# Optimization experiments

Hardware: AMD Instinct MI355X
Metric: run time of the kernel (lower is better)

## Reference

```python
import jax, jax.numpy as jnp
import numpy as np

EMBED = 1024
HEADS = 16
HEAD_DIM = EMBED // HEADS
N, S = 2, 2048


def setup_inputs() -> dict:
    key0 = jax.random.key(0)
    ks = jax.random.split(key0, 9)
    inp = {
        "value": jax.random.normal(ks[0], (N, S, EMBED), dtype=jnp.float32),
        "key": jax.random.normal(ks[1], (N, S, EMBED), dtype=jnp.float32),
        "query": jax.random.normal(ks[2], (N, S, EMBED), dtype=jnp.float32),
        "mask": jax.random.randint(ks[3], (N, 1, S, S), 0, 2, dtype=jnp.int32),
        # per-head projection weights (nn.Linear: y = x @ W.T), bias=False
        "Wv": jax.random.normal(ks[4], (HEAD_DIM, HEAD_DIM), dtype=jnp.float32) / np.sqrt(HEAD_DIM),
        "Wk": jax.random.normal(ks[5], (HEAD_DIM, HEAD_DIM), dtype=jnp.float32) / np.sqrt(HEAD_DIM),
        "Wq": jax.random.normal(ks[6], (HEAD_DIM, HEAD_DIM), dtype=jnp.float32) / np.sqrt(HEAD_DIM),
        "Wo": jax.random.normal(ks[7], (EMBED, EMBED), dtype=jnp.float32) / np.sqrt(EMBED),
        "bo": jax.random.normal(ks[8], (EMBED,), dtype=jnp.float32) * 0.01,
    }
    return inp


def reference(value, key, query, mask, Wv, Wk, Wq, Wo, bo):
    n, q_len = query.shape[0], query.shape[1]
    v = value.reshape(n, -1, HEADS, HEAD_DIM)
    k = key.reshape(n, -1, HEADS, HEAD_DIM)
    q = query.reshape(n, -1, HEADS, HEAD_DIM)
    # per-head linear projections (x @ W.T)
    v = jnp.einsum('nlhd,ed->nlhe', v, Wv)
    k = jnp.einsum('nlhd,ed->nlhe', k, Wk)
    q = jnp.einsum('nlhd,ed->nlhe', q, Wq)
    energy = jnp.einsum('nqhd,nkhd->nhqk', q, k)
    # faithful to the source: masked_fill with +1e20 where mask == 0
    energy = jnp.where(mask == 0, jnp.float32(1e20), energy)
    attention = jax.nn.softmax(energy / jnp.sqrt(jnp.float32(EMBED)), axis=3)
    out = jnp.einsum('nhql,nlhd->nqhd', attention, v)
    out = out.reshape(n, q_len, EMBED)
    return out @ Wo.T + bo
```

## Files before the change

kernel.cpp:

```cpp
#include <hip/hip_runtime.h>
#include <hip/hip_bf16.h>
#include <stdint.h>

#define SEQ 2048

typedef __attribute__((ext_vector_type(8))) short s8v;
typedef __attribute__((ext_vector_type(4))) float f4v;
typedef __attribute__((ext_vector_type(4))) int   i4v;

#define QCLIP 5.5f

static __device__ __forceinline__ unsigned short f2bf(float f) {
  union { float f; unsigned u; } x; x.f = f;
  return (unsigned short)((x.u + 0x7FFFu + ((x.u >> 16) & 1u)) >> 16);
}

static __device__ __forceinline__ void glds16(const void* g, void* l) {
  auto* lp = reinterpret_cast<__attribute__((address_space(3))) unsigned int*>(
      reinterpret_cast<uintptr_t>(l));
  const auto* gp = reinterpret_cast<const __attribute__((address_space(1))) unsigned int*>(
      reinterpret_cast<uintptr_t>(g));
  __builtin_amdgcn_global_load_lds(gp, lp, 16, 0, 0);
}

__global__ void k_prep(const float* __restrict__ V, const float* __restrict__ Wv,
                       const float* __restrict__ Wo,
                       unsigned short* __restrict__ Vb, unsigned short* __restrict__ W2t) {
  const int bid = blockIdx.x, tid = threadIdx.x;
  __shared__ float wv_s[64 * 64];
  if (bid < 2048) {
    int t = bid * 256 + tid;
    const float4* src = (const float4*)V;
    float4 a = src[t * 2], b = src[t * 2 + 1];
    ushort4 p0, p1;
    p0.x = f2bf(a.x); p0.y = f2bf(a.y); p0.z = f2bf(a.z); p0.w = f2bf(a.w);
    p1.x = f2bf(b.x); p1.y = f2bf(b.y); p1.z = f2bf(b.z); p1.w = f2bf(b.w);
    ((ushort4*)Vb)[t * 2] = p0; ((ushort4*)Vb)[t * 2 + 1] = p1;
  } else {
    int b = bid - 2048;
#pragma unroll
    for (int i = 0; i < 4; ++i) { int c = tid + i * 256; ((float4*)wv_s)[c] = ((const float4*)Wv)[c]; }
    __syncthreads();
    const int f = b >> 2;
    const int g = ((b & 3) << 8) + tid;
    const int h = g >> 6, dd = g & 63;
    const float* wo = Wo + f * 1024 + h * 64;
    float acc = 0.f;
#pragma unroll
    for (int e = 0; e < 64; ++e) acc += wv_s[e * 64 + dd] * wo[e];
    W2t[(size_t)f * 1024 + g] = f2bf(acc);
  }
}

__global__ __launch_bounds__(256, 2) void k_gemm0m(
    const unsigned short* __restrict__ A, const unsigned short* __restrict__ Bt,
    signed char* __restrict__ Ut8,
    const int* __restrict__ mask, signed char* __restrict__ Mi8,
    float* __restrict__ rcnt) {
  __shared__ __align__(16) unsigned short As[2][64 * 64];
  __shared__ __align__(16) unsigned short Bs[2][128 * 64];
  const int bid = blockIdx.x, tid = threadIdx.x;

  if (bid >= 512) {
    int row = bid - 512;
    const int4* mrow = (const int4*)(mask + (size_t)row * SEQ);
    int4 a = mrow[tid * 2], b = mrow[tid * 2 + 1];
    unsigned lo = (a.x == 0 ? 1u : 0u) | ((a.y == 0 ? 1u : 0u) << 8) |
                  ((a.z == 0 ? 1u : 0u) << 16) | ((a.w == 0 ? 1u : 0u) << 24);
    unsigned hi = (b.x == 0 ? 1u : 0u) | ((b.y == 0 ? 1u : 0u) << 8) |
                  ((b.z == 0 ? 1u : 0u) << 16) | ((b.w == 0 ? 1u : 0u) << 24);
    uint2 pk; pk.x = lo; pk.y = hi;
    *(uint2*)(Mi8 + (size_t)row * SEQ + tid * 8) = pk;
    int* red = (int*)As;
    red[tid] = (a.x == 0) + (a.y == 0) + (a.z == 0) + (a.w == 0)
             + (b.x == 0) + (b.y == 0) + (b.z == 0) + (b.w == 0);
    __syncthreads();
    for (int s = 128; s > 0; s >>= 1) { if (tid < s) red[tid] += red[tid + s]; __syncthreads(); }
    if (tid == 0) rcnt[row] = 1.0f / (float)red[0];
    return;
  }

  const int Kdim = 1024;
  const int wave = tid >> 6, lane = tid & 63;
  const int quad = lane >> 4, l15 = lane & 15;
  const int wm = (wave & 1) * 32, wn = (wave >> 1) * 64;
  const int lg = ((bid & 7) << 6) + (bid >> 3);
  const int bm0 = (lg >> 3) * 64, bn0 = (lg & 7) * 128;

  const int ra = tid >> 3, pa = tid & 7;
  const unsigned short* ga0 = A + (size_t)(bm0 + ra) * Kdim + (pa ^ ((ra >> 1) & 7)) * 8;
  const unsigned short* ga1 = A + (size_t)(bm0 + 32 + ra) * Kdim + (pa ^ (((ra + 32) >> 1) & 7)) * 8;
  const unsigned short* gb[4];
#pragma unroll
  for (int j = 0; j < 4; ++j) {
    int rb = (tid + j * 256) >> 3;
    gb[j] = Bt + (size_t)(bn0 + rb) * Kdim + ((pa ^ ((rb >> 1) & 7))) * 8;
  }

  f4v acc[2][4];
#pragma unroll
  for (int i = 0; i < 2; ++i)
#pragma unroll
    for (int j = 0; j < 4; ++j) acc[i][j] = (f4v){0.f, 0.f, 0.f, 0.f};

  auto stage = [&](int buf, int k) {
    glds16(ga0 + k, As[buf] + tid * 8);
    glds16(ga1 + k, As[buf] + (tid + 256) * 8);
#pragma unroll
    for (int j = 0; j < 4; ++j) glds16(gb[j] + k, Bs[buf] + (tid + j * 256) * 8);
  };
  auto compute = [&](int buf) {
#pragma unroll
    for (int kg = 0; kg < 2; ++kg) {
      const int pos = ((kg * 4 + quad) ^ ((l15 >> 1) & 7)) * 8;
      s8v af[2], bf[4];
#pragma unroll
      for (int t = 0; t < 2; ++t)
        af[t] = *(const s8v*)(As[buf] + (wm + t * 16 + l15) * 64 + pos);
#pragma unroll
      for (int u = 0; u < 4; ++u)
        bf[u] = *(const s8v*)(Bs[buf] + (wn + u * 16 + l15) * 64 + pos);
#pragma unroll
      for (int tm = 0; tm < 2; ++tm)
#pragma unroll
        for (int tn = 0; tn < 4; ++tn)
          acc[tm][tn] = __builtin_amdgcn_mfma_f32_16x16x32_bf16(af[tm], bf[tn], acc[tm][tn], 0, 0, 0);
    }
  };

  stage(0, 0);
  for (int k0 = 0; k0 < Kdim; k0 += 128) {
    __syncthreads();
    if (k0 + 64 < Kdim) stage(1, k0 + 64);
    compute(0);
    __syncthreads();
    if (k0 + 128 < Kdim) stage(0, k0 + 128);
    compute(1);
  }

  const float qs = 127.0f / QCLIP;
#pragma unroll
  for (int tm = 0; tm < 2; ++tm)
#pragma unroll
    for (int tn = 0; tn < 4; ++tn) {
      int gm0 = bm0 + wm + tm * 16 + quad * 4;
      int f   = bn0 + wn + tn * 16 + l15;
      int batch = gm0 >> 11, l0 = gm0 & 2047;
      unsigned pk = 0;
#pragma unroll
      for (int r = 0; r < 4; ++r) {
        float v = fminf(fmaxf(acc[tm][tn][r], -QCLIP), QCLIP) * qs;
        int q = __float2int_rn(v);
        pk |= ((unsigned)(q & 255)) << (8 * r);
      }
      *(unsigned*)(Ut8 + (size_t)batch * (1024 * SEQ) + (size_t)f * SEQ + l0) = pk;
    }
}

__global__ __launch_bounds__(256, 2) void k_gemm1(
    const signed char* __restrict__ A,
    const signed char* __restrict__ Bt,
    float* __restrict__ Out,
    const float* __restrict__ rcnt, const float* __restrict__ bo) {
  __shared__ __align__(16) signed char As[2][64 * 128];
  __shared__ __align__(16) signed char Bs[2][128 * 128];
  const int bid = blockIdx.x, tid = threadIdx.x;

  const int lg = ((bid & 7) << 6) + (bid >> 3);
  const int batch = lg >> 8;
  const int rest = lg & 255;
  const int bm0 = (rest >> 3) * 64, bn0 = (rest & 7) * 128;

  A    += (size_t)batch * SEQ * SEQ;
  Bt   += (size_t)batch * 1024 * SEQ;
  rcnt += (size_t)batch * SEQ;
  Out  += (size_t)batch * SEQ * 1024;

  const int wave = tid >> 6, lane = tid & 63;
  const int quad = lane >> 4, l15 = lane & 15;
  const int wm = (wave & 1) * 32, wn = (wave >> 1) * 64;

  const signed char* ga[2];
  const signed char* gb[4];
#pragma unroll
  for (int j = 0; j < 2; ++j) {
    int c = tid + j * 256, r = c >> 3, p = c & 7;
    ga[j] = A + (size_t)(bm0 + r) * SEQ + (p ^ ((r >> 1) & 7)) * 16;
  }
#pragma unroll
  for (int j = 0; j < 4; ++j) {
    int c = tid + j * 256, r = c >> 3, p = c & 7;
    gb[j] = Bt + (size_t)(bn0 + r) * SEQ + (p ^ ((r >> 1) & 7)) * 16;
  }

  i4v acc[2][4];
#pragma unroll
  for (int i = 0; i < 2; ++i)
#pragma unroll
    for (int j = 0; j < 4; ++j) acc[i][j] = (i4v){0, 0, 0, 0};

  auto stage = [&](int buf, int k) {
#pragma unroll
    for (int j = 0; j < 2; ++j)
      glds16(ga[j] + k, As[buf] + (tid + j * 256) * 16);
#pragma unroll
    for (int j = 0; j < 4; ++j)
      glds16(gb[j] + k, Bs[buf] + (tid + j * 256) * 16);
  };
  auto compute = [&](int buf) {
#pragma unroll
    for (int kg = 0; kg < 2; ++kg) {
      const int pos = ((kg * 4 + quad) ^ ((l15 >> 1) & 7)) * 16;
      i4v af[2], bf[4];
#pragma unroll
      for (int t = 0; t < 2; ++t)
        af[t] = *(const i4v*)(As[buf] + (wm + t * 16 + l15) * 128 + pos);
#pragma unroll
      for (int u = 0; u < 4; ++u)
        bf[u] = *(const i4v*)(Bs[buf] + (wn + u * 16 + l15) * 128 + pos);
#pragma unroll
      for (int tm = 0; tm < 2; ++tm)
#pragma unroll
        for (int tn = 0; tn < 4; ++tn)
          acc[tm][tn] = __builtin_amdgcn_mfma_i32_16x16x64_i8(af[tm], bf[tn], acc[tm][tn], 0, 0, 0);
    }
  };

  stage(0, 0);
  for (int k0 = 0; k0 < SEQ; k0 += 256) {
    __syncthreads();
    if (k0 + 128 < SEQ) stage(1, k0 + 128);
    compute(0);
    __syncthreads();
    if (k0 + 256 < SEQ) stage(0, k0 + 256);
    compute(1);
  }

  const float s = QCLIP / 127.0f;
#pragma unroll
  for (int tm = 0; tm < 2; ++tm)
#pragma unroll
    for (int tn = 0; tn < 4; ++tn) {
      int gm0 = bm0 + wm + tm * 16 + quad * 4;
      int f   = bn0 + wn + tn * 16 + l15;
      float bof = bo[f];
#pragma unroll
      for (int r = 0; r < 4; ++r) {
        int row = gm0 + r;
        Out[(size_t)row * 1024 + f] = (float)acc[tm][tn][r] * s * rcnt[row] + bof;
      }
    }
}

extern "C" void kernel_launch(void* const* d_in, const int* in_sizes, int n_in,
                              void* d_out, int out_size, void* d_ws, size_t ws_size,
                              hipStream_t stream) {
  const float* V   = (const float*)d_in[0];
  const int* mask  = (const int*)d_in[3];
  const float* Wv  = (const float*)d_in[4];
  const float* Wo  = (const float*)d_in[7];
  const float* bo  = (const float*)d_in[8];

  char* ws = (char*)d_ws;
  unsigned short* W2t  = (unsigned short*)ws;
  signed char*    Ut8  = (signed char*)(ws + ((size_t)2  << 20));
  unsigned short* Vb   = (unsigned short*)(ws + ((size_t)6  << 20));
  signed char*    Mi8  = (signed char*)(ws + ((size_t)14 << 20));
  float*          rcnt = (float*)(ws + ((size_t)22 << 20));

  k_prep<<<6144, 256, 0, stream>>>(V, Wv, Wo, Vb, W2t);
  k_gemm0m<<<4608, 256, 0, stream>>>(Vb, W2t, Ut8, mask, Mi8, rcnt);
  k_gemm1<<<512, 256, 0, stream>>>(Mi8, Ut8, (float*)d_out, rcnt, bo);
}
```

Measured before the change: 156.7 us.

## Fuse fp32-to-bf16 conversion of V into the GEMM A-tile loading

```diff
diff --git a/kernel.cpp b/kernel.cpp
--- a/kernel.cpp
+++ b/kernel.cpp
@@ -23,37 +23,31 @@
   __builtin_amdgcn_global_load_lds(gp, lp, 16, 0, 0);
 }
 
-__global__ void k_prep(const float* __restrict__ V, const float* __restrict__ Wv,
-                       const float* __restrict__ Wo,
-                       unsigned short* __restrict__ Vb, unsigned short* __restrict__ W2t) {
-  const int bid = blockIdx.x, tid = threadIdx.x;
+__global__ void k_prepW(const float* __restrict__ Wv, const float* __restrict__ Wo,
+                        unsigned short* __restrict__ W2t) {
+  const int f = blockIdx.x, tid = threadIdx.x;
   __shared__ float wv_s[64 * 64];
-  if (bid < 2048) {
-    int t = bid * 256 + tid;
-    const float4* src = (const float4*)V;
-    float4 a = src[t * 2], b = src[t * 2 + 1];
-    ushort4 p0, p1;
-    p0.x = f2bf(a.x); p0.y = f2bf(a.y); p0.z = f2bf(a.z); p0.w = f2bf(a.w);
-    p1.x = f2bf(b.x); p1.y = f2bf(b.y); p1.z = f2bf(b.z); p1.w = f2bf(b.w);
-    ((ushort4*)Vb)[t * 2] = p0; ((ushort4*)Vb)[t * 2 + 1] = p1;
-  } else {
-    int b = bid - 2048;
-#pragma unroll
-    for (int i = 0; i < 4; ++i) { int c = tid + i * 256; ((float4*)wv_s)[c] = ((const float4*)Wv)[c]; }
-    __syncthreads();
-    const int f = b >> 2;
-    const int g = ((b & 3) << 8) + tid;
-    const int h = g >> 6, dd = g & 63;
-    const float* wo = Wo + f * 1024 + h * 64;
+  __shared__ float wo_s[1024];
+#pragma unroll
+  for (int i = 0; i < 4; ++i) {
+    int c = tid + i * 256;
+    ((float4*)wv_s)[c] = ((const float4*)Wv)[c];
+  }
+  ((float4*)wo_s)[tid] = ((const float4*)(Wo + (size_t)f * 1024))[tid];
+  __syncthreads();
+#pragma unroll
+  for (int gg = 0; gg < 4; ++gg) {
+    int g = gg * 256 + tid;
+    int dd = g & 63, h = g >> 6;
     float acc = 0.f;
 #pragma unroll
-    for (int e = 0; e < 64; ++e) acc += wv_s[e * 64 + dd] * wo[e];
+    for (int e = 0; e < 64; ++e) acc += wv_s[e * 64 + dd] * wo_s[h * 64 + e];
     W2t[(size_t)f * 1024 + g] = f2bf(acc);
   }
 }
 
 __global__ __launch_bounds__(256, 2) void k_gemm0m(
-    const unsigned short* __restrict__ A, const unsigned short* __restrict__ Bt,
+    const float* __restrict__ V, const unsigned short* __restrict__ Bt,
     signed char* __restrict__ Ut8,
     const int* __restrict__ mask, signed char* __restrict__ Mi8,
     float* __restrict__ rcnt) {
@@ -87,14 +81,17 @@
   const int lg = ((bid & 7) << 6) + (bid >> 3);
   const int bm0 = (lg >> 3) * 64, bn0 = (lg & 7) * 128;
 
-  const int ra = tid >> 3, pa = tid & 7;
-  const unsigned short* ga0 = A + (size_t)(bm0 + ra) * Kdim + (pa ^ ((ra >> 1) & 7)) * 8;
-  const unsigned short* ga1 = A + (size_t)(bm0 + 32 + ra) * Kdim + (pa ^ (((ra + 32) >> 1) & 7)) * 8;
+  const float* gva[2];
+#pragma unroll
+  for (int j = 0; j < 2; ++j) {
+    int c = tid + j * 256, r = c >> 3, p = c & 7;
+    gva[j] = V + (size_t)(bm0 + r) * 1024 + (p ^ ((r >> 1) & 7)) * 8;
+  }
   const unsigned short* gb[4];
 #pragma unroll
   for (int j = 0; j < 4; ++j) {
     int rb = (tid + j * 256) >> 3;
-    gb[j] = Bt + (size_t)(bn0 + rb) * Kdim + ((pa ^ ((rb >> 1) & 7))) * 8;
+    gb[j] = Bt + (size_t)(bn0 + rb) * Kdim + ((tid & 7) ^ ((rb >> 1) & 7)) * 8;
   }
 
   f4v acc[2][4];
@@ -103,9 +100,26 @@
 #pragma unroll
     for (int j = 0; j < 4; ++j) acc[i][j] = (f4v){0.f, 0.f, 0.f, 0.f};
 
-  auto stage = [&](int buf, int k) {
-    glds16(ga0 + k, As[buf] + tid * 8);
-    glds16(ga1 + k, As[buf] + (tid + 256) * 8);
+  float4 rA[2][2];
+  auto loadA = [&](int k) {
+#pragma unroll
+    for (int j = 0; j < 2; ++j) {
+      rA[j][0] = *(const float4*)(gva[j] + k);
+      rA[j][1] = *(const float4*)(gva[j] + k + 4);
+    }
+  };
+  auto writeA = [&](int buf) {
+#pragma unroll
+    for (int j = 0; j < 2; ++j) {
+      s8v pk;
+      pk[0] = (short)f2bf(rA[j][0].x); pk[1] = (short)f2bf(rA[j][0].y);
+      pk[2] = (short)f2bf(rA[j][0].z); pk[3] = (short)f2bf(rA[j][0].w);
+      pk[4] = (short)f2bf(rA[j][1].x); pk[5] = (short)f2bf(rA[j][1].y);
+      pk[6] = (short)f2bf(rA[j][1].z); pk[7] = (short)f2bf(rA[j][1].w);
+      *(s8v*)(As[buf] + (tid + j * 256) * 8) = pk;
+    }
+  };
+  auto stageB = [&](int buf, int k) {
 #pragma unroll
     for (int j = 0; j < 4; ++j) glds16(gb[j] + k, Bs[buf] + (tid + j * 256) * 8);
   };
@@ -128,14 +142,16 @@
     }
   };
 
-  stage(0, 0);
+  stageB(0, 0); loadA(0); writeA(0);
   for (int k0 = 0; k0 < Kdim; k0 += 128) {
     __syncthreads();
-    if (k0 + 64 < Kdim) stage(1, k0 + 64);
+    if (k0 + 64 < Kdim) { loadA(k0 + 64); stageB(1, k0 + 64); }
     compute(0);
-    __syncthreads();
-    if (k0 + 128 < Kdim) stage(0, k0 + 128);
+    if (k0 + 64 < Kdim) writeA(1);
+    __syncthreads();
+    if (k0 + 128 < Kdim) { loadA(k0 + 128); stageB(0, k0 + 128); }
     compute(1);
+    if (k0 + 128 < Kdim) writeA(0);
   }
 
   const float qs = 127.0f / QCLIP;
@@ -264,11 +280,10 @@
   char* ws = (char*)d_ws;
   unsigned short* W2t  = (unsigned short*)ws;
   signed char*    Ut8  = (signed char*)(ws + ((size_t)2  << 20));
-  unsigned short* Vb   = (unsigned short*)(ws + ((size_t)6  << 20));
   signed char*    Mi8  = (signed char*)(ws + ((size_t)14 << 20));
   float*          rcnt = (float*)(ws + ((size_t)22 << 20));
 
-  k_prep<<<6144, 256, 0, stream>>>(V, Wv, Wo, Vb, W2t);
-  k_gemm0m<<<4608, 256, 0, stream>>>(Vb, W2t, Ut8, mask, Mi8, rcnt);
+  k_prepW<<<1024, 256, 0, stream>>>(Wv, Wo, W2t);
+  k_gemm0m<<<4608, 256, 0, stream>>>(V, W2t, Ut8, mask, Mi8, rcnt);
   k_gemm1<<<512, 256, 0, stream>>>(Mi8, Ut8, (float*)d_out, rcnt, bo);
 }
```

After: 160.3 us. 2.3% more time.
